# Performance work log

Measured on AMD Instinct MI355X. Metric: run time of the kernel, lower is better.

## Reference

```python
import jax, jax.numpy as jnp
import numpy as np

N_NODES = 20000
N_EDGES = 320000
N_GRAPHS = 64
IN_DIM = 39
HID = 128
HEADS = 4
NUM_CONV = 3
PRED_HID = 32
N_TASKS = 1
NEG_SLOPE = 0.2


def setup_inputs() -> dict:
    key = jax.random.key(0)
    ks = jax.random.split(key, 16)
    node_feat = jax.random.normal(ks[0], (N_NODES, IN_DIM), dtype=jnp.float32)
    edge_index = jax.random.randint(ks[1], (2, N_EDGES), 0, N_NODES, dtype=jnp.int64)
    batch = jnp.sort(jax.random.randint(ks[2], (N_NODES,), 0, N_GRAPHS, dtype=jnp.int64))
    s = 0.05
    return {
        "node_feat": node_feat,
        "edge_index": edge_index,
        "batch": batch,
        "emb_W": jax.random.normal(ks[3], (IN_DIM, HID), dtype=jnp.float32) * s,
        "emb_b": jnp.zeros((HID,), dtype=jnp.float32),
        "lin_W": jax.random.normal(ks[4], (NUM_CONV, HID, HEADS * HID), dtype=jnp.float32) * s,
        "att_src": jax.random.normal(ks[5], (NUM_CONV, HEADS, HID), dtype=jnp.float32) * s,
        "att_dst": jax.random.normal(ks[6], (NUM_CONV, HEADS, HID), dtype=jnp.float32) * s,
        "conv_b": jnp.zeros((NUM_CONV, HID), dtype=jnp.float32),
        "fc_W": jax.random.normal(ks[7], (HID, PRED_HID), dtype=jnp.float32) * s,
        "fc_b": jnp.zeros((PRED_HID,), dtype=jnp.float32),
        "out_W": jax.random.normal(ks[8], (PRED_HID, N_TASKS), dtype=jnp.float32) * s,
        "out_b": jnp.zeros((N_TASKS,), dtype=jnp.float32),
    }


def _gat_layer(x, src, dst, W, a_src, a_dst, b):
    # PyG GATConv (concat=False): per-head projection, additive attention,
    # segment softmax over incoming edges of each target node, head-mean + bias.
    N = x.shape[0]
    h = (x @ W).reshape(N, HEADS, HID)            # [N, H, F]
    a_s = jnp.einsum('nhf,hf->nh', h, a_src)       # [N, H]
    a_d = jnp.einsum('nhf,hf->nh', h, a_dst)       # [N, H]
    e = jax.nn.leaky_relu(a_s[src] + a_d[dst], NEG_SLOPE)   # [E, H]
    e_max = jax.ops.segment_max(e, dst, num_segments=N)      # [N, H]
    e = jnp.exp(e - e_max[dst])
    denom = jax.ops.segment_sum(e, dst, num_segments=N)      # [N, H]
    alpha = e / denom[dst]                                    # [E, H]
    msg = h[src] * alpha[..., None]                           # [E, H, F]
    out = jax.ops.segment_sum(msg, dst, num_segments=N)      # [N, H, F]
    return out.mean(axis=1) + b                               # [N, F]


def reference(node_feat, edge_index, batch, emb_W, emb_b, lin_W, att_src, att_dst,
              conv_b, fc_W, fc_b, out_W, out_b):
    N = node_feat.shape[0]
    loops = jnp.arange(N, dtype=edge_index.dtype)
    src = jnp.concatenate([edge_index[0], loops])  # add_self_loops=True
    dst = jnp.concatenate([edge_index[1], loops])

    x = node_feat @ emb_W + emb_b
    for l in range(NUM_CONV):
        x = _gat_layer(x, src, dst, lin_W[l], att_src[l], att_dst[l], conv_b[l])

    # global_mean_pool
    sums = jax.ops.segment_sum(x, batch, num_segments=N_GRAPHS)              # [G, F]
    cnt = jax.ops.segment_sum(jnp.ones((N,), x.dtype), batch, num_segments=N_GRAPHS)
    g = sums / jnp.maximum(cnt, 1.0)[:, None]

    g = g @ fc_W + fc_b
    return g @ out_W + out_b
```

## Files before the change

### kernel.cpp

```cpp
#include <hip/hip_runtime.h>
#include <math.h>

#define N_NODES 20000
#define E0      320000
#define E_TOT   (E0 + N_NODES)
#define N_GRAPHS 64
#define IN_DIM  39
#define HID     128
#define HEADS   4
#define HHID    (HEADS * HID)
#define NUM_CONV 3
#define PRED_HID 32
#define NEG_SLOPE 0.2f

__device__ __forceinline__ int esrc(const int* __restrict__ ei, int e) {
    return e < E0 ? ei[e] : (e - E0);
}
__device__ __forceinline__ int edst(const int* __restrict__ ei, int e) {
    return e < E0 ? ei[E0 + e] : (e - E0);
}

__global__ void k_deg(const int* __restrict__ ei, int* __restrict__ deg) {
    int e = blockIdx.x * blockDim.x + threadIdx.x;
    if (e >= E_TOT) return;
    atomicAdd(&deg[edst(ei, e)], 1);
}

__global__ __launch_bounds__(1024) void k_scan(const int* __restrict__ deg,
                                               int* __restrict__ row_ptr,
                                               int* __restrict__ cursor) {
    __shared__ int part[1024];
    const int CHUNK = 20;
    int t = threadIdx.x;
    int base = t * CHUNK;
    int s = 0;
    for (int i = 0; i < CHUNK; i++) {
        int idx = base + i;
        if (idx < N_NODES) s += deg[idx];
    }
    part[t] = s;
    __syncthreads();
    for (int off = 1; off < 1024; off <<= 1) {
        int v = (t >= off) ? part[t - off] : 0;
        __syncthreads();
        part[t] += v;
        __syncthreads();
    }
    int run = part[t] - s;
    for (int i = 0; i < CHUNK; i++) {
        int idx = base + i;
        if (idx < N_NODES) {
            row_ptr[idx] = run;
            cursor[idx]  = run;
            run += deg[idx];
        }
    }
    if (t == 1023) row_ptr[N_NODES] = part[1023];
}

__global__ void k_scatter(const int* __restrict__ ei, int* __restrict__ cursor,
                          int* __restrict__ csr_src, int* __restrict__ csr_dst) {
    int e = blockIdx.x * blockDim.x + threadIdx.x;
    if (e >= E_TOT) return;
    int d = edst(ei, e);
    int pos = atomicAdd(&cursor[d], 1);
    csr_src[pos] = esrc(ei, e);
    csr_dst[pos] = d;
}

__global__ __launch_bounds__(128) void k_emb(const float* __restrict__ nf,
                                             const float* __restrict__ W,
                                             const float* __restrict__ b,
                                             float* __restrict__ x) {
    __shared__ float f[IN_DIM];
    int n = blockIdx.x, t = threadIdx.x;
    if (t < IN_DIM) f[t] = nf[(size_t)n * IN_DIM + t];
    __syncthreads();
    float acc = b[t];
#pragma unroll
    for (int k = 0; k < IN_DIM; k++) acc += f[k] * W[k * HID + t];
    x[(size_t)n * HID + t] = acc;
}

__global__ __launch_bounds__(128) void k_wsd(const float* __restrict__ lin_W,
                                             const float* __restrict__ attS,
                                             const float* __restrict__ attD,
                                             float* __restrict__ Wsd) {
    int l = blockIdx.x >> 3, j = blockIdx.x & 7, k = threadIdx.x;
    int h = j & 3;
    const float* Wl = lin_W + (size_t)l * HID * HHID;
    const float* av = ((j < 4) ? attS : attD) + ((size_t)l * HEADS + h) * HID;
    const float* wr = Wl + (size_t)k * HHID + h * HID;
    float dot = 0.f;
#pragma unroll 4
    for (int f = 0; f < HID; f++) dot += wr[f] * av[f];
    Wsd[(size_t)l * 8 * HID + j * HID + k] = dot;
}

__global__ __launch_bounds__(256) void k_attproj(const float* __restrict__ x,
                                                 const float* __restrict__ WsdL,
                                                 float* __restrict__ A8) {
    __shared__ float sW[8 * HID];
    for (int i = threadIdx.x; i < 8 * HID; i += 256) sW[i] = WsdL[i];
    __syncthreads();
    int wid = threadIdx.x >> 6, lane = threadIdx.x & 63;
    int n = blockIdx.x * 4 + wid;
    if (n >= N_NODES) return;
    float2 xv = *(const float2*)(x + (size_t)n * HID + lane * 2);
    float p[8];
#pragma unroll
    for (int j = 0; j < 8; j++) {
        float v = xv.x * sW[j * HID + lane * 2] + xv.y * sW[j * HID + lane * 2 + 1];
#pragma unroll
        for (int off = 32; off; off >>= 1) v += __shfl_xor(v, off, 64);
        p[j] = v;
    }
    if (lane == 0) {
        *(float4*)(A8 + (size_t)n * 8)     = make_float4(p[0], p[1], p[2], p[3]);
        *(float4*)(A8 + (size_t)n * 8 + 4) = make_float4(p[4], p[5], p[6], p[7]);
    }
}

__global__ void k_edge(const int* __restrict__ csr_src, const int* __restrict__ csr_dst,
                       const float* __restrict__ A8, float* __restrict__ expE) {
    int j = blockIdx.x * blockDim.x + threadIdx.x;
    if (j >= E_TOT) return;
    int s = csr_src[j], d = csr_dst[j];
    float4 vs = *(const float4*)(A8 + (size_t)s * 8);
    float4 vd = *(const float4*)(A8 + (size_t)d * 8 + 4);
    float4 r;
    float v;
    v = vs.x + vd.x; v = v > 0.f ? v : NEG_SLOPE * v; r.x = expf(v);
    v = vs.y + vd.y; v = v > 0.f ? v : NEG_SLOPE * v; r.y = expf(v);
    v = vs.z + vd.z; v = v > 0.f ? v : NEG_SLOPE * v; r.z = expf(v);
    v = vs.w + vd.w; v = v > 0.f ? v : NEG_SLOPE * v; r.w = expf(v);
    *(float4*)(expE + (size_t)j * HEADS) = r;
}

__global__ __launch_bounds__(256) void k_aggr(const float* __restrict__ x,
                                              const int* __restrict__ row_ptr,
                                              const int* __restrict__ csr_src,
                                              const float* __restrict__ expE,
                                              float* __restrict__ agg) {
    int wid = threadIdx.x >> 6, lane = threadIdx.x & 63;
    int n = blockIdx.x * 4 + wid;
    if (n >= N_NODES) return;
    int beg = row_ptr[n], end = row_ptr[n + 1];
    float a0x = 0.f, a0y = 0.f, a1x = 0.f, a1y = 0.f;
    float a2x = 0.f, a2y = 0.f, a3x = 0.f, a3y = 0.f;
    float d0 = 0.f, d1 = 0.f, d2 = 0.f, d3 = 0.f;
    int s_cur = (beg < end) ? csr_src[beg] : 0;
    for (int i = beg; i < end; i++) {
        int s_nx = (i + 1 < end) ? csr_src[i + 1] : 0;
        float4 ep = *(const float4*)(expE + (size_t)i * HEADS);
        float2 xv = *(const float2*)(x + (size_t)s_cur * HID + lane * 2);
        a0x += ep.x * xv.x; a0y += ep.x * xv.y;
        a1x += ep.y * xv.x; a1y += ep.y * xv.y;
        a2x += ep.z * xv.x; a2y += ep.z * xv.y;
        a3x += ep.w * xv.x; a3y += ep.w * xv.y;
        d0 += ep.x; d1 += ep.y; d2 += ep.z; d3 += ep.w;
        s_cur = s_nx;
    }
    float i0 = 1.f / d0, i1 = 1.f / d1, i2 = 1.f / d2, i3 = 1.f / d3;
    float* ag = agg + (size_t)n * HHID;
    *(float2*)(ag + 0 * HID + lane * 2) = make_float2(a0x * i0, a0y * i0);
    *(float2*)(ag + 1 * HID + lane * 2) = make_float2(a1x * i1, a1y * i1);
    *(float2*)(ag + 2 * HID + lane * 2) = make_float2(a2x * i2, a2y * i2);
    *(float2*)(ag + 3 * HID + lane * 2) = make_float2(a3x * i3, a3y * i3);
}

#define G2_BM 32
#define G2_BK 64
#define G2_LDAT 36
__global__ __launch_bounds__(256) void k_gemm2(const float* __restrict__ agg,
                                               const float* __restrict__ W,
                                               const float* __restrict__ bias,
                                               float* __restrict__ xn, int M) {
    __shared__ float At[G2_BK][G2_LDAT];
    __shared__ float Bs[G2_BK][HID];
    int tid = threadIdx.x;
    int row0 = blockIdx.x * G2_BM;
    int ty = tid >> 4, tx = tid & 15;
    int r0 = ty * 2, c0 = tx * 4;
    float acc[2][8] = {};

    for (int kt = 0; kt < HHID / G2_BK; kt++) {
        __syncthreads();
#pragma unroll
        for (int i = 0; i < 2; i++) {
            int idx = tid + i * 256;
            int r = idx >> 4;
            int c4 = idx & 15;
            int gr = row0 + r;
            float4 v = make_float4(0.f, 0.f, 0.f, 0.f);
            if (gr < M) v = *(const float4*)(agg + (size_t)gr * HHID + kt * G2_BK + c4 * 4);
            At[c4 * 4 + 0][r] = v.x;
            At[c4 * 4 + 1][r] = v.y;
            At[c4 * 4 + 2][r] = v.z;
            At[c4 * 4 + 3][r] = v.w;
        }
#pragma unroll
        for (int i = 0; i < 8; i++) {
            int idx = tid + i * 256;
            int kr = idx >> 5;
            int c4 = idx & 31;
            int kg = kt * G2_BK + kr;
            int hd = kg >> 7, kk = kg & 127;
            float4 v = *(const float4*)(W + (size_t)kk * HHID + hd * HID + c4 * 4);
            *(float4*)(&Bs[kr][c4 * 4]) = v;
        }
        __syncthreads();
#pragma unroll 8
        for (int k = 0; k < G2_BK; k++) {
            float2 av = *(float2*)(&At[k][r0]);
            float4 b1 = *(float4*)(&Bs[k][c0]);
            float4 b2 = *(float4*)(&Bs[k][c0 + 64]);
            acc[0][0] += av.x * b1.x; acc[0][1] += av.x * b1.y; acc[0][2] += av.x * b1.z; acc[0][3] += av.x * b1.w;
            acc[0][4] += av.x * b2.x; acc[0][5] += av.x * b2.y; acc[0][6] += av.x * b2.z; acc[0][7] += av.x * b2.w;
            acc[1][0] += av.y * b1.x; acc[1][1] += av.y * b1.y; acc[1][2] += av.y * b1.z; acc[1][3] += av.y * b1.w;
            acc[1][4] += av.y * b2.x; acc[1][5] += av.y * b2.y; acc[1][6] += av.y * b2.z; acc[1][7] += av.y * b2.w;
        }
    }
    float4 bb1 = *(const float4*)(bias + c0);
    float4 bb2 = *(const float4*)(bias + c0 + 64);
#pragma unroll
    for (int i = 0; i < 2; i++) {
        int gr = row0 + r0 + i;
        if (gr < M) {
            float4 v1 = make_float4(0.25f * acc[i][0] + bb1.x, 0.25f * acc[i][1] + bb1.y,
                                    0.25f * acc[i][2] + bb1.z, 0.25f * acc[i][3] + bb1.w);
            float4 v2 = make_float4(0.25f * acc[i][4] + bb2.x, 0.25f * acc[i][5] + bb2.y,
                                    0.25f * acc[i][6] + bb2.z, 0.25f * acc[i][7] + bb2.w);
            *(float4*)(xn + (size_t)gr * HID + c0)      = v1;
            *(float4*)(xn + (size_t)gr * HID + c0 + 64) = v2;
        }
    }
}

#define POOL_NPB 64
__global__ __launch_bounds__(128) void k_pool(const float* __restrict__ x,
                                              const int* __restrict__ batch,
                                              float* __restrict__ g_sum,
                                              int* __restrict__ g_cnt) {
    int t = threadIdx.x;
    int n0 = blockIdx.x * POOL_NPB;
    int n1 = n0 + POOL_NPB; if (n1 > N_NODES) n1 = N_NODES;
    if (n0 >= n1) return;
    int cur = batch[n0];
    float acc = 0.f;
    int cnt = 0;
    for (int n = n0; n < n1; n++) {
        int b = batch[n];
        if (b != cur) {
            atomicAdd(&g_sum[cur * HID + t], acc);
            if (t == 0) atomicAdd(&g_cnt[cur], cnt);
            acc = 0.f; cnt = 0; cur = b;
        }
        acc += x[(size_t)n * HID + t];
        cnt++;
    }
    atomicAdd(&g_sum[cur * HID + t], acc);
    if (t == 0) atomicAdd(&g_cnt[cur], cnt);
}

__global__ __launch_bounds__(64) void k_head(const float* __restrict__ g_sum,
                                             const int* __restrict__ g_cnt,
                                             const float* __restrict__ fcW,
                                             const float* __restrict__ fcb,
                                             const float* __restrict__ outW,
                                             const float* __restrict__ outb,
                                             float* __restrict__ out) {
    int g = blockIdx.x, t = threadIdx.x;
    float inv = 1.f / fmaxf((float)g_cnt[g], 1.f);
    float val = 0.f;
    if (t < PRED_HID) {
        float dot = fcb[t];
        for (int f = 0; f < HID; f++)
            dot += (g_sum[g * HID + f] * inv) * fcW[f * PRED_HID + t];
        val = dot * outW[t];
    }
#pragma unroll
    for (int off = 32; off; off >>= 1) val += __shfl_xor(val, off, 64);
    if (t == 0) out[g] = val + outb[0];
}

extern "C" void kernel_launch(void* const* d_in, const int* in_sizes, int n_in,
                              void* d_out, int out_size, void* d_ws, size_t ws_size,
                              hipStream_t stream) {
    const float* node_feat = (const float*)d_in[0];
    const int*   edge_index = (const int*)d_in[1];
    const int*   batch     = (const int*)d_in[2];
    const float* emb_W     = (const float*)d_in[3];
    const float* emb_b     = (const float*)d_in[4];
    const float* lin_W     = (const float*)d_in[5];
    const float* att_src   = (const float*)d_in[6];
    const float* att_dst   = (const float*)d_in[7];
    const float* conv_b    = (const float*)d_in[8];
    const float* fc_W      = (const float*)d_in[9];
    const float* fc_b      = (const float*)d_in[10];
    const float* out_W     = (const float*)d_in[11];
    const float* out_b     = (const float*)d_in[12];
    float* out = (float*)d_out;

    char* p = (char*)d_ws;
    auto alloc = [&](size_t bytes) {
        void* r = (void*)p;
        p += (bytes + 255) & ~(size_t)255;
        return r;
    };
    float* x0      = (float*)alloc((size_t)N_NODES * HID * 4);
    float* x1      = (float*)alloc((size_t)N_NODES * HID * 4);
    float* agg     = (float*)alloc((size_t)N_NODES * HHID * 4);
    float* A8      = (float*)alloc((size_t)N_NODES * 8 * 4);
    float* Wsd     = (float*)alloc((size_t)NUM_CONV * 8 * HID * 4);
    float* expE    = (float*)alloc((size_t)E_TOT * HEADS * 4);
    int*   deg     = (int*)alloc((size_t)(N_NODES + 1) * 4);
    int*   row_ptr = (int*)alloc((size_t)(N_NODES + 1) * 4);
    int*   cursor  = (int*)alloc((size_t)N_NODES * 4);
    int*   csr_src = (int*)alloc((size_t)E_TOT * 4);
    int*   csr_dst = (int*)alloc((size_t)E_TOT * 4);
    float* g_sum   = (float*)alloc((size_t)N_GRAPHS * HID * 4);
    int*   g_cnt   = (int*)alloc((size_t)N_GRAPHS * 4);

    const int EB = (E_TOT + 255) / 256;
    const int NB4 = (N_NODES + 3) / 4;

    hipMemsetAsync(deg, 0, (size_t)N_NODES * 4, stream);
    k_deg<<<EB, 256, 0, stream>>>(edge_index, deg);
    k_scan<<<1, 1024, 0, stream>>>(deg, row_ptr, cursor);
    k_scatter<<<EB, 256, 0, stream>>>(edge_index, cursor, csr_src, csr_dst);

    k_wsd<<<NUM_CONV * 8, 128, 0, stream>>>(lin_W, att_src, att_dst, Wsd);

    k_emb<<<N_NODES, 128, 0, stream>>>(node_feat, emb_W, emb_b, x0);

    float* xin = x0;
    float* xout = x1;
    for (int l = 0; l < NUM_CONV; l++) {
        const float* Wl = lin_W + (size_t)l * HID * HHID;
        const float* bl = conv_b + (size_t)l * HID;
        k_attproj<<<NB4, 256, 0, stream>>>(xin, Wsd + (size_t)l * 8 * HID, A8);
        k_edge<<<EB, 256, 0, stream>>>(csr_src, csr_dst, A8, expE);
        k_aggr<<<NB4, 256, 0, stream>>>(xin, row_ptr, csr_src, expE, agg);
        k_gemm2<<<(N_NODES + G2_BM - 1) / G2_BM, 256, 0, stream>>>(agg, Wl, bl, xout, N_NODES);
        float* tmp = xin; xin = xout; xout = tmp;
    }

    hipMemsetAsync(g_sum, 0, (size_t)N_GRAPHS * HID * 4, stream);
    hipMemsetAsync(g_cnt, 0, (size_t)N_GRAPHS * 4, stream);
    k_pool<<<(N_NODES + POOL_NPB - 1) / POOL_NPB, 128, 0, stream>>>(xin, batch, g_sum, g_cnt);
    k_head<<<N_GRAPHS, 64, 0, stream>>>(g_sum, g_cnt, fc_W, fc_b,
                                        out_W, out_b, out);
}
```

Before: 482.6 us.

## Fuse edge softmax into aggregation, split-K GEMM, fuse attention projection into finalize

Removes the separate edge kernel and expE buffer by computing the leaky-relu and exp for each edge inside the aggregation loop, reading the per-node attention scores directly. This also drops csr_dst from CSR construction. The projection GEMM becomes split-K over heads with larger 64-row tiles, a swizzled shared-memory A layout and 4x8 register tiles. A new finalize kernel sums the partials, applies the bias and computes the next layer's attention projections, so the standalone attproj launch per layer goes away. The cost is recomputing exp per edge inside the aggregation and extra partial-buffer traffic.

```diff
diff --git a/kernel.cpp b/kernel.cpp
--- a/kernel.cpp
+++ b/kernel.cpp
@@ -59,13 +59,12 @@
 }
 
 __global__ void k_scatter(const int* __restrict__ ei, int* __restrict__ cursor,
-                          int* __restrict__ csr_src, int* __restrict__ csr_dst) {
+                          int* __restrict__ csr_src) {
     int e = blockIdx.x * blockDim.x + threadIdx.x;
     if (e >= E_TOT) return;
     int d = edst(ei, e);
     int pos = atomicAdd(&cursor[d], 1);
     csr_src[pos] = esrc(ei, e);
-    csr_dst[pos] = d;
 }
 
 __global__ __launch_bounds__(128) void k_emb(const float* __restrict__ nf,
@@ -121,30 +120,15 @@
     }
 }
 
-__global__ void k_edge(const int* __restrict__ csr_src, const int* __restrict__ csr_dst,
-                       const float* __restrict__ A8, float* __restrict__ expE) {
-    int j = blockIdx.x * blockDim.x + threadIdx.x;
-    if (j >= E_TOT) return;
-    int s = csr_src[j], d = csr_dst[j];
-    float4 vs = *(const float4*)(A8 + (size_t)s * 8);
-    float4 vd = *(const float4*)(A8 + (size_t)d * 8 + 4);
-    float4 r;
-    float v;
-    v = vs.x + vd.x; v = v > 0.f ? v : NEG_SLOPE * v; r.x = expf(v);
-    v = vs.y + vd.y; v = v > 0.f ? v : NEG_SLOPE * v; r.y = expf(v);
-    v = vs.z + vd.z; v = v > 0.f ? v : NEG_SLOPE * v; r.z = expf(v);
-    v = vs.w + vd.w; v = v > 0.f ? v : NEG_SLOPE * v; r.w = expf(v);
-    *(float4*)(expE + (size_t)j * HEADS) = r;
-}
-
 __global__ __launch_bounds__(256) void k_aggr(const float* __restrict__ x,
                                               const int* __restrict__ row_ptr,
                                               const int* __restrict__ csr_src,
-                                              const float* __restrict__ expE,
+                                              const float* __restrict__ A8,
                                               float* __restrict__ agg) {
     int wid = threadIdx.x >> 6, lane = threadIdx.x & 63;
     int n = blockIdx.x * 4 + wid;
     if (n >= N_NODES) return;
+    float4 vd = *(const float4*)(A8 + (size_t)n * 8 + 4);
     int beg = row_ptr[n], end = row_ptr[n + 1];
     float a0x = 0.f, a0y = 0.f, a1x = 0.f, a1y = 0.f;
     float a2x = 0.f, a2y = 0.f, a3x = 0.f, a3y = 0.f;
@@ -152,13 +136,17 @@
     int s_cur = (beg < end) ? csr_src[beg] : 0;
     for (int i = beg; i < end; i++) {
         int s_nx = (i + 1 < end) ? csr_src[i + 1] : 0;
-        float4 ep = *(const float4*)(expE + (size_t)i * HEADS);
+        float4 vs = *(const float4*)(A8 + (size_t)s_cur * 8);
         float2 xv = *(const float2*)(x + (size_t)s_cur * HID + lane * 2);
-        a0x += ep.x * xv.x; a0y += ep.x * xv.y;
-        a1x += ep.y * xv.x; a1y += ep.y * xv.y;
-        a2x += ep.z * xv.x; a2y += ep.z * xv.y;
-        a3x += ep.w * xv.x; a3y += ep.w * xv.y;
-        d0 += ep.x; d1 += ep.y; d2 += ep.z; d3 += ep.w;
+        float v0 = vs.x + vd.x; v0 = fmaxf(v0, NEG_SLOPE * v0); float e0 = expf(v0);
+        float v1 = vs.y + vd.y; v1 = fmaxf(v1, NEG_SLOPE * v1); float e1 = expf(v1);
+        float v2 = vs.z + vd.z; v2 = fmaxf(v2, NEG_SLOPE * v2); float e2 = expf(v2);
+        float v3 = vs.w + vd.w; v3 = fmaxf(v3, NEG_SLOPE * v3); float e3 = expf(v3);
+        a0x += e0 * xv.x; a0y += e0 * xv.y;
+        a1x += e1 * xv.x; a1y += e1 * xv.y;
+        a2x += e2 * xv.x; a2y += e2 * xv.y;
+        a3x += e3 * xv.x; a3y += e3 * xv.y;
+        d0 += e0; d1 += e1; d2 += e2; d3 += e3;
         s_cur = s_nx;
     }
     float i0 = 1.f / d0, i1 = 1.f / d1, i2 = 1.f / d2, i3 = 1.f / d3;
@@ -169,71 +157,110 @@
     *(float2*)(ag + 3 * HID + lane * 2) = make_float2(a3x * i3, a3y * i3);
 }
 
-#define G2_BM 32
-#define G2_BK 64
-#define G2_LDAT 36
+#define G2_BM 64
+#define G2_KSPLIT 4
 __global__ __launch_bounds__(256) void k_gemm2(const float* __restrict__ agg,
                                                const float* __restrict__ W,
-                                               const float* __restrict__ bias,
-                                               float* __restrict__ xn, int M) {
-    __shared__ float At[G2_BK][G2_LDAT];
-    __shared__ float Bs[G2_BK][HID];
+                                               float* __restrict__ part, int M) {
+    __shared__ float At[64][G2_BM];
+    __shared__ float Bs[64][HID];
     int tid = threadIdx.x;
     int row0 = blockIdx.x * G2_BM;
+    int ks = blockIdx.y;
     int ty = tid >> 4, tx = tid & 15;
-    int r0 = ty * 2, c0 = tx * 4;
-    float acc[2][8] = {};
-
-    for (int kt = 0; kt < HHID / G2_BK; kt++) {
+    int r0 = ty * 4, c0 = tx * 4;
+    float acc[4][8] = {};
+
+#pragma unroll
+    for (int kt = 0; kt < 2; kt++) {
+        int kbase = ks * 128 + kt * 64;
         __syncthreads();
 #pragma unroll
-        for (int i = 0; i < 2; i++) {
+        for (int i = 0; i < 4; i++) {
             int idx = tid + i * 256;
             int r = idx >> 4;
             int c4 = idx & 15;
             int gr = row0 + r;
             float4 v = make_float4(0.f, 0.f, 0.f, 0.f);
-            if (gr < M) v = *(const float4*)(agg + (size_t)gr * HHID + kt * G2_BK + c4 * 4);
-            At[c4 * 4 + 0][r] = v.x;
-            At[c4 * 4 + 1][r] = v.y;
-            At[c4 * 4 + 2][r] = v.z;
-            At[c4 * 4 + 3][r] = v.w;
+            if (gr < M) v = *(const float4*)(agg + (size_t)gr * HHID + kbase + c4 * 4);
+            int sw = (((r >> 2) ^ c4) << 2) + (r & 3);
+            At[c4 * 4 + 0][sw] = v.x;
+            At[c4 * 4 + 1][sw] = v.y;
+            At[c4 * 4 + 2][sw] = v.z;
+            At[c4 * 4 + 3][sw] = v.w;
         }
 #pragma unroll
         for (int i = 0; i < 8; i++) {
             int idx = tid + i * 256;
             int kr = idx >> 5;
             int c4 = idx & 31;
-            int kg = kt * G2_BK + kr;
+            int kg = kbase + kr;
             int hd = kg >> 7, kk = kg & 127;
-            float4 v = *(const float4*)(W + (size_t)kk * HHID + hd * HID + c4 * 4);
-            *(float4*)(&Bs[kr][c4 * 4]) = v;
+            *(float4*)(&Bs[kr][c4 * 4]) =
+                *(const float4*)(W + (size_t)kk * HHID + hd * HID + c4 * 4);
         }
         __syncthreads();
-#pragma unroll 8
-        for (int k = 0; k < G2_BK; k++) {
-            float2 av = *(float2*)(&At[k][r0]);
+#pragma unroll 4
+        for (int k = 0; k < 64; k++) {
+            float4 av = *(float4*)(&At[k][((ty ^ (k >> 2)) << 2)]);
             float4 b1 = *(float4*)(&Bs[k][c0]);
             float4 b2 = *(float4*)(&Bs[k][c0 + 64]);
             acc[0][0] += av.x * b1.x; acc[0][1] += av.x * b1.y; acc[0][2] += av.x * b1.z; acc[0][3] += av.x * b1.w;
             acc[0][4] += av.x * b2.x; acc[0][5] += av.x * b2.y; acc[0][6] += av.x * b2.z; acc[0][7] += av.x * b2.w;
             acc[1][0] += av.y * b1.x; acc[1][1] += av.y * b1.y; acc[1][2] += av.y * b1.z; acc[1][3] += av.y * b1.w;
             acc[1][4] += av.y * b2.x; acc[1][5] += av.y * b2.y; acc[1][6] += av.y * b2.z; acc[1][7] += av.y * b2.w;
-        }
-    }
-    float4 bb1 = *(const float4*)(bias + c0);
-    float4 bb2 = *(const float4*)(bias + c0 + 64);
-#pragma unroll
-    for (int i = 0; i < 2; i++) {
+            acc[2][0] += av.z * b1.x; acc[2][1] += av.z * b1.y; acc[2][2] += av.z * b1.z; acc[2][3] += av.z * b1.w;
+            acc[2][4] += av.z * b2.x; acc[2][5] += av.z * b2.y; acc[2][6] += av.z * b2.z; acc[2][7] += av.z * b2.w;
+            acc[3][0] += av.w * b1.x; acc[3][1] += av.w * b1.y; acc[3][2] += av.w * b1.z; acc[3][3] += av.w * b1.w;
+            acc[3][4] += av.w * b2.x; acc[3][5] += av.w * b2.y; acc[3][6] += av.w * b2.z; acc[3][7] += av.w * b2.w;
+        }
+    }
+    float* pb = part + (size_t)ks * M * HID;
+#pragma unroll
+    for (int i = 0; i < 4; i++) {
         int gr = row0 + r0 + i;
         if (gr < M) {
-            float4 v1 = make_float4(0.25f * acc[i][0] + bb1.x, 0.25f * acc[i][1] + bb1.y,
-                                    0.25f * acc[i][2] + bb1.z, 0.25f * acc[i][3] + bb1.w);
-            float4 v2 = make_float4(0.25f * acc[i][4] + bb2.x, 0.25f * acc[i][5] + bb2.y,
-                                    0.25f * acc[i][6] + bb2.z, 0.25f * acc[i][7] + bb2.w);
-            *(float4*)(xn + (size_t)gr * HID + c0)      = v1;
-            *(float4*)(xn + (size_t)gr * HID + c0 + 64) = v2;
-        }
+            *(float4*)(pb + (size_t)gr * HID + c0) =
+                make_float4(acc[i][0], acc[i][1], acc[i][2], acc[i][3]);
+            *(float4*)(pb + (size_t)gr * HID + c0 + 64) =
+                make_float4(acc[i][4], acc[i][5], acc[i][6], acc[i][7]);
+        }
+    }
+}
+
+__global__ __launch_bounds__(256) void k_gfin(const float* __restrict__ part,
+                                              const float* __restrict__ bias,
+                                              const float* __restrict__ WsdL,
+                                              float* __restrict__ xn,
+                                              float* __restrict__ A8, int M) {
+    __shared__ float sW[8 * HID];
+    for (int i = threadIdx.x; i < 8 * HID; i += 256) sW[i] = WsdL[i];
+    __syncthreads();
+    int wid = threadIdx.x >> 6, lane = threadIdx.x & 63;
+    int n = blockIdx.x * 4 + wid;
+    if (n >= M) return;
+    size_t off = (size_t)n * HID + lane * 2;
+    size_t str = (size_t)M * HID;
+    float2 p0 = *(const float2*)(part + off);
+    float2 p1 = *(const float2*)(part + str + off);
+    float2 p2 = *(const float2*)(part + 2 * str + off);
+    float2 p3 = *(const float2*)(part + 3 * str + off);
+    float2 bb = *(const float2*)(bias + lane * 2);
+    float2 xv;
+    xv.x = 0.25f * (p0.x + p1.x + p2.x + p3.x) + bb.x;
+    xv.y = 0.25f * (p0.y + p1.y + p2.y + p3.y) + bb.y;
+    *(float2*)(xn + off) = xv;
+    float p[8];
+#pragma unroll
+    for (int j = 0; j < 8; j++) {
+        float v = xv.x * sW[j * HID + lane * 2] + xv.y * sW[j * HID + lane * 2 + 1];
+#pragma unroll
+        for (int o = 32; o; o >>= 1) v += __shfl_xor(v, o, 64);
+        p[j] = v;
+    }
+    if (lane == 0) {
+        *(float4*)(A8 + (size_t)n * 8)     = make_float4(p[0], p[1], p[2], p[3]);
+        *(float4*)(A8 + (size_t)n * 8 + 4) = make_float4(p[4], p[5], p[6], p[7]);
     }
 }
 
@@ -311,14 +338,13 @@
     float* x0      = (float*)alloc((size_t)N_NODES * HID * 4);
     float* x1      = (float*)alloc((size_t)N_NODES * HID * 4);
     float* agg     = (float*)alloc((size_t)N_NODES * HHID * 4);
+    float* part    = (float*)alloc((size_t)G2_KSPLIT * N_NODES * HID * 4);
     float* A8      = (float*)alloc((size_t)N_NODES * 8 * 4);
     float* Wsd     = (float*)alloc((size_t)NUM_CONV * 8 * HID * 4);
-    float* expE    = (float*)alloc((size_t)E_TOT * HEADS * 4);
     int*   deg     = (int*)alloc((size_t)(N_NODES + 1) * 4);
     int*   row_ptr = (int*)alloc((size_t)(N_NODES + 1) * 4);
     int*   cursor  = (int*)alloc((size_t)N_NODES * 4);
     int*   csr_src = (int*)alloc((size_t)E_TOT * 4);
-    int*   csr_dst = (int*)alloc((size_t)E_TOT * 4);
     float* g_sum   = (float*)alloc((size_t)N_GRAPHS * HID * 4);
     int*   g_cnt   = (int*)alloc((size_t)N_GRAPHS * 4);
 
@@ -328,21 +354,25 @@
     hipMemsetAsync(deg, 0, (size_t)N_NODES * 4, stream);
     k_deg<<<EB, 256, 0, stream>>>(edge_index, deg);
     k_scan<<<1, 1024, 0, stream>>>(deg, row_ptr, cursor);
-    k_scatter<<<EB, 256, 0, stream>>>(edge_index, cursor, csr_src, csr_dst);
+    k_scatter<<<EB, 256, 0, stream>>>(edge_index, cursor, csr_src);
 
     k_wsd<<<NUM_CONV * 8, 128, 0, stream>>>(lin_W, att_src, att_dst, Wsd);
 
     k_emb<<<N_NODES, 128, 0, stream>>>(node_feat, emb_W, emb_b, x0);
+    k_attproj<<<NB4, 256, 0, stream>>>(x0, Wsd, A8);
 
     float* xin = x0;
     float* xout = x1;
     for (int l = 0; l < NUM_CONV; l++) {
         const float* Wl = lin_W + (size_t)l * HID * HHID;
         const float* bl = conv_b + (size_t)l * HID;
-        k_attproj<<<NB4, 256, 0, stream>>>(xin, Wsd + (size_t)l * 8 * HID, A8);
-        k_edge<<<EB, 256, 0, stream>>>(csr_src, csr_dst, A8, expE);
-        k_aggr<<<NB4, 256, 0, stream>>>(xin, row_ptr, csr_src, expE, agg);
-        k_gemm2<<<(N_NODES + G2_BM - 1) / G2_BM, 256, 0, stream>>>(agg, Wl, bl, xout, N_NODES);
+        int lnext = (l + 1 < NUM_CONV) ? l + 1 : NUM_CONV - 1;
+
+        k_aggr<<<NB4, 256, 0, stream>>>(xin, row_ptr, csr_src, A8, agg);
+        dim3 gg((N_NODES + G2_BM - 1) / G2_BM, G2_KSPLIT);
+        k_gemm2<<<gg, 256, 0, stream>>>(agg, Wl, part, N_NODES);
+        k_gfin<<<NB4, 256, 0, stream>>>(part, bl, Wsd + (size_t)lnext * 8 * HID,
+                                        xout, A8, N_NODES);
         float* tmp = xin; xin = xout; xout = tmp;
     }
 
```

Result: no change. 480.3 us (-0.5%).
